# Kernel tuning notes

Measured on AMD Instinct MI355X. Metric: run time of the kernel, lower is better.

Reference implementation:

```python
import jax, jax.numpy as jnp
import numpy as np


def _l2norm(x):
    # matches torch F.normalize(p=2, dim=-1) with eps clamp
    return x / jnp.clip(jnp.linalg.norm(x, axis=-1, keepdims=True), 1e-12)


def setup_inputs() -> dict:
    key = jax.random.key(0)
    k1, k2 = jax.random.split(key)
    I, J, S, H = 32, 32, 256, 768
    return {
        "query_embs": jax.random.normal(k1, (I, S, H), dtype=jnp.float32),
        "key_embs": jax.random.normal(k2, (J, S, H), dtype=jnp.float32),
        "q_mask": jnp.ones((I, S), dtype=jnp.float32),
        "k_mask": jnp.ones((J, S), dtype=jnp.float32),
        "alpha_raw": jnp.asarray(0.5, dtype=jnp.float32),  # learned scalar param
    }


def reference(query_embs, key_embs, q_mask, k_mask, alpha_raw):
    # eval path: gumbel_temp=None, use_max=False, do_distance=True, exp_decay=True
    S = query_embs.shape[1]
    pos = jnp.arange(S)
    distance = jnp.abs(pos[:, None] - pos[None, :]).astype(jnp.float32)  # [S, S]
    alpha = jax.nn.softplus(alpha_raw)

    qn = _l2norm(query_embs)  # [I, S, H]
    kn = _l2norm(key_embs)    # [J, T, H]

    # cross similarity [I, J, S, T] with exponential distance decay
    sim = jnp.einsum('ish,jth->ijst', qn, kn) * jnp.exp(-alpha * distance)

    # valid pair mask [I, J, S, T]
    valid = q_mask[:, None, :, None] * k_mask[None, :, None, :]
    masked = sim * valid - (1.0 - valid) * 1e9

    p = jax.nn.softmax(masked, axis=-1)             # softmax over key tokens t
    agg = jnp.einsum('ijst,jth->ijsh', p, kn)       # soft-aligned key embedding
    scores = jnp.einsum('ish,ijsh->ijs', qn, agg)   # per-query-token score
    scores = scores * q_mask[:, None, :]
    denom = jnp.clip(jnp.sum(q_mask, axis=-1, keepdims=True), 1.0)  # [I, 1]
    return jnp.sum(scores, axis=-1) / denom         # [I, J]
```

## Files before the change

kernel.cpp:

```cpp
#include <hip/hip_runtime.h>

#define I_DIM 32
#define J_DIM 32
#define S_DIM 256
#define H_DIM 768
#define KC    32
#define NCH   (H_DIM / KC)
#define TILE_B 32768
#define WSQ_BYTES ((size_t)I_DIM * NCH * TILE_B)
#define WSK_BYTES ((size_t)J_DIM * NCH * TILE_B)

typedef _Float16 f16x8 __attribute__((ext_vector_type(8)));
typedef float    f32x16 __attribute__((ext_vector_type(16)));

static __device__ __forceinline__ unsigned short f16bits(_Float16 h) {
    union { _Float16 f; unsigned short u; } cv; cv.f = h; return cv.u;
}

__global__ __launch_bounds__(256) void li_split_kernel(
    const float* __restrict__ qe, const float* __restrict__ ke,
    char* __restrict__ wsQ, char* __restrict__ wsK)
{
    const int lane = threadIdx.x & 63;
    const int w    = threadIdx.x >> 6;
    const int r    = blockIdx.x * 4 + w;
    const bool isQ = r < I_DIM * S_DIM;
    const int row  = isQ ? r : r - I_DIM * S_DIM;
    const float* base = (isQ ? qe : ke) + (size_t)row * H_DIM;

    float4 v[3];
    v[0] = *(const float4*)(base + 4 * lane);
    v[1] = *(const float4*)(base + 4 * lane + 256);
    v[2] = *(const float4*)(base + 4 * lane + 512);
    float ss = 0.0f;
    #pragma unroll
    for (int g = 0; g < 3; ++g)
        ss += v[g].x * v[g].x + v[g].y * v[g].y + v[g].z * v[g].z + v[g].w * v[g].w;
    #pragma unroll
    for (int m = 1; m < 64; m <<= 1) ss += __shfl_xor(ss, m, 64);
    const float inv = 1.0f / fmaxf(sqrtf(ss), 1e-12f);

    const int mi  = row >> 8;
    const int s   = row & 255;
    const int r7  = s & 7;
    char* wsb = (isQ ? wsQ : wsK) + (size_t)mi * NCH * TILE_B + s * 128;

    #pragma unroll
    for (int g = 0; g < 3; ++g) {
        const int k0 = 4 * lane + 256 * g;
        const int c  = k0 >> 5;
        const int kk = k0 & 31;
        float xn[4] = {v[g].x * inv, v[g].y * inv, v[g].z * inv, v[g].w * inv};
        unsigned short hb[4], lb[4];
        #pragma unroll
        for (int e = 0; e < 4; ++e) {
            _Float16 h  = (_Float16)xn[e];
            _Float16 lo = (_Float16)(xn[e] - (float)h);
            hb[e] = f16bits(h);
            lb[e] = f16bits(lo);
        }
        char* p = wsb + (size_t)c * TILE_B + (((kk >> 3) ^ r7) << 4) + (kk & 7) * 2;
        *(uint2*)(p)        = make_uint2(hb[0] | ((unsigned)hb[1] << 16), hb[2] | ((unsigned)hb[3] << 16));
        *(uint2*)((char*)((size_t)p ^ 64)) = make_uint2(lb[0] | ((unsigned)lb[1] << 16), lb[2] | ((unsigned)lb[3] << 16));
    }
}

__global__ __launch_bounds__(512, 2) void li_mfma_kernel(
    const char* __restrict__ wsQ, const char* __restrict__ wsK,
    const float* __restrict__ qm, const float* __restrict__ km,
    const float* __restrict__ alpha_raw, float* __restrict__ out)
{
    __shared__ __align__(16) char sQ[2][TILE_B];
    __shared__ __align__(16) char sK[2][TILE_B];
    __shared__ float kmsh[256], qmsh[256];
    __shared__ float pm[256][2], pL[256][2], pW[256][2];
    __shared__ float redA[512], redB[512];

    const int tid = threadIdx.x;
    const int wid = tid >> 6;
    const int l   = tid & 63;
    const int l31 = l & 31;
    const int hi  = l >> 5;
    const int wx  = wid & 1;
    const int wy  = wid >> 1;
    const int r7  = l31 & 7;

    const int bidx = blockIdx.x;
    const int x  = bidx & 7;
    const int r0 = bidx >> 3;
    const int j  = x * 4 + (r0 & 3);
    const int i  = r0 >> 2;

    if (tid < 256) {
        kmsh[tid] = km[j * 256 + tid];
        qmsh[tid] = qm[i * 256 + tid];
    }
    const float araw  = alpha_raw[0];
    const float alpha = (araw > 20.0f) ? araw : log1pf(expf(araw));
    const float nal   = -alpha;

    const char* qbase = wsQ + (size_t)i * NCH * TILE_B;
    const char* kbase = wsK + (size_t)j * NCH * TILE_B;

    f32x16 acc[2][4];
    #pragma unroll
    for (int mr = 0; mr < 2; ++mr)
        #pragma unroll
        for (int nt = 0; nt < 4; ++nt)
            #pragma unroll
            for (int z = 0; z < 16; ++z) acc[mr][nt][z] = 0.0f;

#define STAGE(buf, c)                                                                      \
    do {                                                                                   \
        const char* qt_ = qbase + (size_t)(c) * TILE_B + wid * 4096 + l * 16;              \
        const char* kt_ = kbase + (size_t)(c) * TILE_B + wid * 4096 + l * 16;              \
        char* dq_ = sQ[buf] + wid * 4096;                                                  \
        char* dk_ = sK[buf] + wid * 4096;                                                  \
        _Pragma("unroll")                                                                  \
        for (int u = 0; u < 4; ++u)                                                        \
            __builtin_amdgcn_global_load_lds(                                              \
                (const __attribute__((address_space(1))) void*)(qt_ + u * 1024),           \
                (__attribute__((address_space(3))) void*)(dq_ + u * 1024), 16, 0, 0);      \
        _Pragma("unroll")                                                                  \
        for (int u = 0; u < 4; ++u)                                                        \
            __builtin_amdgcn_global_load_lds(                                              \
                (const __attribute__((address_space(1))) void*)(kt_ + u * 1024),           \
                (__attribute__((address_space(3))) void*)(dk_ + u * 1024), 16, 0, 0);      \
    } while (0)

    STAGE(0, 0);
    __syncthreads();

    for (int c = 0; c < NCH; ++c) {
        if (c + 1 < NCH) STAGE((c + 1) & 1, c + 1);
        const char* bQ = sQ[c & 1];
        const char* bK = sK[c & 1];
        #pragma unroll
        for (int ks = 0; ks < 2; ++ks) {
            const int soff = ((ks * 2 + hi) ^ r7) << 4;
            const int rA = wy * 64 + l31;
            const int rB = rA + 32;
            const f16x8 qhA = *(const f16x8*)(bQ + rA * 128 + soff);
            const f16x8 qlA = *(const f16x8*)(bQ + ((rA * 128 + soff) ^ 64));
            const f16x8 qhB = *(const f16x8*)(bQ + rB * 128 + soff);
            const f16x8 qlB = *(const f16x8*)(bQ + ((rB * 128 + soff) ^ 64));
            f16x8 kh[4], kl[4];
            #pragma unroll
            for (int nt = 0; nt < 4; ++nt) {
                const int rk = wx * 128 + nt * 32 + l31;
                kh[nt] = *(const f16x8*)(bK + rk * 128 + soff);
                kl[nt] = *(const f16x8*)(bK + ((rk * 128 + soff) ^ 64));
            }
            #pragma unroll
            for (int nt = 0; nt < 4; ++nt) {
                acc[0][nt] = __builtin_amdgcn_mfma_f32_32x32x16_f16(qhA, kh[nt], acc[0][nt], 0, 0, 0);
                acc[1][nt] = __builtin_amdgcn_mfma_f32_32x32x16_f16(qhB, kh[nt], acc[1][nt], 0, 0, 0);
            }
            #pragma unroll
            for (int nt = 0; nt < 4; ++nt) {
                acc[0][nt] = __builtin_amdgcn_mfma_f32_32x32x16_f16(qhA, kl[nt], acc[0][nt], 0, 0, 0);
                acc[1][nt] = __builtin_amdgcn_mfma_f32_32x32x16_f16(qhB, kl[nt], acc[1][nt], 0, 0, 0);
            }
            #pragma unroll
            for (int nt = 0; nt < 4; ++nt) {
                acc[0][nt] = __builtin_amdgcn_mfma_f32_32x32x16_f16(qlA, kh[nt], acc[0][nt], 0, 0, 0);
                acc[1][nt] = __builtin_amdgcn_mfma_f32_32x32x16_f16(qlB, kh[nt], acc[1][nt], 0, 0, 0);
            }
        }
        __syncthreads();
    }
#undef STAGE

    #pragma unroll
    for (int mrep = 0; mrep < 2; ++mrep) {
        #pragma unroll
        for (int reg = 0; reg < 16; ++reg) {
            const int srow = wy * 64 + mrep * 32 + hi * 4 + (reg & 3) + 8 * (reg >> 2);
            const float qms = qmsh[srow];
            float mv[4], cvv[4];
            float mloc = -3.0e38f;
            #pragma unroll
            for (int nt = 0; nt < 4; ++nt) {
                const int tcol = wx * 128 + nt * 32 + l31;
                const float cv = acc[mrep][nt][reg];
                int dd = srow - tcol; dd = dd < 0 ? -dd : dd;
                const float valid = qms * kmsh[tcol];
                const float m = cv * __expf(nal * (float)dd) * valid - (1.0f - valid) * 1e9f;
                mv[nt] = m; cvv[nt] = cv;
                mloc = fmaxf(mloc, m);
            }
            #pragma unroll
            for (int mm = 1; mm < 32; mm <<= 1)
                mloc = fmaxf(mloc, __shfl_xor(mloc, mm, 32));
            float L = 0.0f, W = 0.0f;
            #pragma unroll
            for (int nt = 0; nt < 4; ++nt) {
                const float e = __expf(mv[nt] - mloc);
                L += e;
                W += e * cvv[nt];
            }
            #pragma unroll
            for (int mm = 1; mm < 32; mm <<= 1) {
                L += __shfl_xor(L, mm, 32);
                W += __shfl_xor(W, mm, 32);
            }
            if (l31 == 0) {
                pm[srow][wx] = mloc;
                pL[srow][wx] = L;
                pW[srow][wx] = W;
            }
        }
    }
    __syncthreads();

    float contrib = 0.0f, qq = 0.0f;
    if (tid < 256) {
        const float m0 = pm[tid][0], m1 = pm[tid][1];
        const float M  = fmaxf(m0, m1);
        const float e0 = __expf(m0 - M), e1 = __expf(m1 - M);
        const float L  = pL[tid][0] * e0 + pL[tid][1] * e1;
        const float W  = pW[tid][0] * e0 + pW[tid][1] * e1;
        contrib = (W / L) * qmsh[tid];
        qq = qmsh[tid];
    }
    redA[tid] = contrib;
    redB[tid] = qq;
    __syncthreads();
    for (int off = 256; off > 0; off >>= 1) {
        if (tid < off) {
            redA[tid] += redA[tid + off];
            redB[tid] += redB[tid + off];
        }
        __syncthreads();
    }
    if (tid == 0) out[i * 32 + j] = redA[0] / fmaxf(redB[0], 1.0f);
}

extern "C" void kernel_launch(void* const* d_in, const int* in_sizes, int n_in,
                              void* d_out, int out_size, void* d_ws, size_t ws_size,
                              hipStream_t stream)
{
    const float* qe = (const float*)d_in[0];
    const float* ke = (const float*)d_in[1];
    const float* qm = (const float*)d_in[2];
    const float* km = (const float*)d_in[3];
    const float* al = (const float*)d_in[4];
    float* out = (float*)d_out;

    char* wsQ = (char*)d_ws;
    char* wsK = wsQ + WSQ_BYTES;

    hipLaunchKernelGGL(li_split_kernel, dim3((I_DIM + J_DIM) * S_DIM / 4), dim3(256),
                       0, stream, qe, ke, wsQ, wsK);
    hipLaunchKernelGGL(li_mfma_kernel, dim3(I_DIM * J_DIM), dim3(512), 0, stream,
                       wsQ, wsK, qm, km, al, out);
}
```

Measured before the change: 416.3 us.

## Interleave prefetch loads with MFMA phases using explicit barriers and priority

Restructures the main split-f16 GEMM loop into four phases per K-chunk. Each phase issues one slice of the next chunk's global-to-LDS loads, then LDS reads and a batch of 12 MFMAs. Explicit s_waitcnt, sched_barrier and s_barrier calls control ordering, and s_setprio raises priority around the MFMA bursts. The aim is to spread memory traffic across the compute and cut register pressure by loading only two K tiles at a time. It adds many more barriers per chunk, which could cost synchronisation overhead.

```diff
diff --git a/kernel.cpp b/kernel.cpp
--- a/kernel.cpp
+++ b/kernel.cpp
@@ -110,66 +110,121 @@
             #pragma unroll
             for (int z = 0; z < 16; ++z) acc[mr][nt][z] = 0.0f;
 
-#define STAGE(buf, c)                                                                      \
-    do {                                                                                   \
-        const char* qt_ = qbase + (size_t)(c) * TILE_B + wid * 4096 + l * 16;              \
-        const char* kt_ = kbase + (size_t)(c) * TILE_B + wid * 4096 + l * 16;              \
-        char* dq_ = sQ[buf] + wid * 4096;                                                  \
-        char* dk_ = sK[buf] + wid * 4096;                                                  \
-        _Pragma("unroll")                                                                  \
-        for (int u = 0; u < 4; ++u)                                                        \
-            __builtin_amdgcn_global_load_lds(                                              \
-                (const __attribute__((address_space(1))) void*)(qt_ + u * 1024),           \
-                (__attribute__((address_space(3))) void*)(dq_ + u * 1024), 16, 0, 0);      \
-        _Pragma("unroll")                                                                  \
-        for (int u = 0; u < 4; ++u)                                                        \
-            __builtin_amdgcn_global_load_lds(                                              \
-                (const __attribute__((address_space(1))) void*)(kt_ + u * 1024),           \
-                (__attribute__((address_space(3))) void*)(dk_ + u * 1024), 16, 0, 0);      \
+    const int sgo = wid * 4096 + l * 16;
+
+#define GLL2(buf, c, u)                                                                   \
+    do {                                                                                  \
+        __builtin_amdgcn_global_load_lds(                                                 \
+            (const __attribute__((address_space(1))) void*)                               \
+                (qbase + (size_t)(c) * TILE_B + sgo + (u) * 1024),                        \
+            (__attribute__((address_space(3))) void*)(sQ[buf] + wid * 4096 + (u) * 1024), \
+            16, 0, 0);                                                                    \
+        __builtin_amdgcn_global_load_lds(                                                 \
+            (const __attribute__((address_space(1))) void*)                               \
+                (kbase + (size_t)(c) * TILE_B + sgo + (u) * 1024),                        \
+            (__attribute__((address_space(3))) void*)(sK[buf] + wid * 4096 + (u) * 1024), \
+            16, 0, 0);                                                                    \
     } while (0)
 
-    STAGE(0, 0);
-    __syncthreads();
+#define SB() __builtin_amdgcn_sched_barrier(0)
+#define BAR() do { SB(); __builtin_amdgcn_s_barrier(); SB(); } while (0)
+#define LGKM0() do { asm volatile("s_waitcnt lgkmcnt(0)" ::: "memory"); SB(); } while (0)
+#define MFMA1(A, B, C) __builtin_amdgcn_mfma_f32_32x32x16_f16(A, B, C, 0, 0, 0)
+
+#define MFMA12(KHa, KLa, KHb, KLb, na, nb)                          \
+    do {                                                            \
+        __builtin_amdgcn_s_setprio(1);                              \
+        acc[0][na] = MFMA1(qh0, KHa, acc[0][na]);                   \
+        acc[0][nb] = MFMA1(qh0, KHb, acc[0][nb]);                   \
+        acc[1][na] = MFMA1(qh1, KHa, acc[1][na]);                   \
+        acc[1][nb] = MFMA1(qh1, KHb, acc[1][nb]);                   \
+        acc[0][na] = MFMA1(qh0, KLa, acc[0][na]);                   \
+        acc[0][nb] = MFMA1(qh0, KLb, acc[0][nb]);                   \
+        acc[1][na] = MFMA1(qh1, KLa, acc[1][na]);                   \
+        acc[1][nb] = MFMA1(qh1, KLb, acc[1][nb]);                   \
+        acc[0][na] = MFMA1(ql0, KHa, acc[0][na]);                   \
+        acc[0][nb] = MFMA1(ql0, KHb, acc[0][nb]);                   \
+        acc[1][na] = MFMA1(ql1, KHa, acc[1][na]);                   \
+        acc[1][nb] = MFMA1(ql1, KHb, acc[1][nb]);                   \
+        __builtin_amdgcn_s_setprio(0);                              \
+    } while (0)
+
+    const int rqA = (wy * 64 + l31) * 128;
+    const int rqB = rqA + 32 * 128;
+    const int rk0 = (wx * 128 + l31) * 128;
+
+    GLL2(0, 0, 0); GLL2(0, 0, 1); GLL2(0, 0, 2); GLL2(0, 0, 3);
+    asm volatile("s_waitcnt vmcnt(0)" ::: "memory");
+    BAR();
 
     for (int c = 0; c < NCH; ++c) {
-        if (c + 1 < NCH) STAGE((c + 1) & 1, c + 1);
         const char* bQ = sQ[c & 1];
         const char* bK = sK[c & 1];
-        #pragma unroll
-        for (int ks = 0; ks < 2; ++ks) {
-            const int soff = ((ks * 2 + hi) ^ r7) << 4;
-            const int rA = wy * 64 + l31;
-            const int rB = rA + 32;
-            const f16x8 qhA = *(const f16x8*)(bQ + rA * 128 + soff);
-            const f16x8 qlA = *(const f16x8*)(bQ + ((rA * 128 + soff) ^ 64));
-            const f16x8 qhB = *(const f16x8*)(bQ + rB * 128 + soff);
-            const f16x8 qlB = *(const f16x8*)(bQ + ((rB * 128 + soff) ^ 64));
-            f16x8 kh[4], kl[4];
-            #pragma unroll
-            for (int nt = 0; nt < 4; ++nt) {
-                const int rk = wx * 128 + nt * 32 + l31;
-                kh[nt] = *(const f16x8*)(bK + rk * 128 + soff);
-                kl[nt] = *(const f16x8*)(bK + ((rk * 128 + soff) ^ 64));
-            }
-            #pragma unroll
-            for (int nt = 0; nt < 4; ++nt) {
-                acc[0][nt] = __builtin_amdgcn_mfma_f32_32x32x16_f16(qhA, kh[nt], acc[0][nt], 0, 0, 0);
-                acc[1][nt] = __builtin_amdgcn_mfma_f32_32x32x16_f16(qhB, kh[nt], acc[1][nt], 0, 0, 0);
-            }
-            #pragma unroll
-            for (int nt = 0; nt < 4; ++nt) {
-                acc[0][nt] = __builtin_amdgcn_mfma_f32_32x32x16_f16(qhA, kl[nt], acc[0][nt], 0, 0, 0);
-                acc[1][nt] = __builtin_amdgcn_mfma_f32_32x32x16_f16(qhB, kl[nt], acc[1][nt], 0, 0, 0);
-            }
-            #pragma unroll
-            for (int nt = 0; nt < 4; ++nt) {
-                acc[0][nt] = __builtin_amdgcn_mfma_f32_32x32x16_f16(qlA, kh[nt], acc[0][nt], 0, 0, 0);
-                acc[1][nt] = __builtin_amdgcn_mfma_f32_32x32x16_f16(qlB, kh[nt], acc[1][nt], 0, 0, 0);
-            }
-        }
-        __syncthreads();
-    }
-#undef STAGE
+        const int nb = (c + 1) & 1;
+        const bool pf = (c + 1 < NCH);
+
+        f16x8 qh0, ql0, qh1, ql1;
+        f16x8 kh_a, kl_a, kh_b, kl_b;
+
+        {
+            const int soff = (hi ^ r7) << 4;
+            if (pf) {
+                GLL2(nb, c + 1, 0);
+                asm volatile("s_waitcnt vmcnt(2)" ::: "memory");
+            } else {
+                asm volatile("s_waitcnt vmcnt(0)" ::: "memory");
+            }
+            BAR();
+            qh0 = *(const f16x8*)(bQ + rqA + soff);
+            ql0 = *(const f16x8*)(bQ + ((rqA + soff) ^ 64));
+            qh1 = *(const f16x8*)(bQ + rqB + soff);
+            ql1 = *(const f16x8*)(bQ + ((rqB + soff) ^ 64));
+            kh_a = *(const f16x8*)(bK + rk0 + soff);
+            kl_a = *(const f16x8*)(bK + ((rk0 + soff) ^ 64));
+            kh_b = *(const f16x8*)(bK + rk0 + 32 * 128 + soff);
+            kl_b = *(const f16x8*)(bK + ((rk0 + 32 * 128 + soff) ^ 64));
+            LGKM0();
+            MFMA12(kh_a, kl_a, kh_b, kl_b, 0, 1);
+            BAR();
+            if (pf) GLL2(nb, c + 1, 1);
+            kh_a = *(const f16x8*)(bK + rk0 + 64 * 128 + soff);
+            kl_a = *(const f16x8*)(bK + ((rk0 + 64 * 128 + soff) ^ 64));
+            kh_b = *(const f16x8*)(bK + rk0 + 96 * 128 + soff);
+            kl_b = *(const f16x8*)(bK + ((rk0 + 96 * 128 + soff) ^ 64));
+            BAR();
+            LGKM0();
+            MFMA12(kh_a, kl_a, kh_b, kl_b, 2, 3);
+            BAR();
+        }
+        {
+            const int soff = ((2 + hi) ^ r7) << 4;
+            if (pf) GLL2(nb, c + 1, 2);
+            qh0 = *(const f16x8*)(bQ + rqA + soff);
+            ql0 = *(const f16x8*)(bQ + ((rqA + soff) ^ 64));
+            qh1 = *(const f16x8*)(bQ + rqB + soff);
+            ql1 = *(const f16x8*)(bQ + ((rqB + soff) ^ 64));
+            kh_a = *(const f16x8*)(bK + rk0 + soff);
+            kl_a = *(const f16x8*)(bK + ((rk0 + soff) ^ 64));
+            kh_b = *(const f16x8*)(bK + rk0 + 32 * 128 + soff);
+            kl_b = *(const f16x8*)(bK + ((rk0 + 32 * 128 + soff) ^ 64));
+            BAR();
+            LGKM0();
+            MFMA12(kh_a, kl_a, kh_b, kl_b, 0, 1);
+            BAR();
+            if (pf) GLL2(nb, c + 1, 3);
+            kh_a = *(const f16x8*)(bK + rk0 + 64 * 128 + soff);
+            kl_a = *(const f16x8*)(bK + ((rk0 + 64 * 128 + soff) ^ 64));
+            kh_b = *(const f16x8*)(bK + rk0 + 96 * 128 + soff);
+            kl_b = *(const f16x8*)(bK + ((rk0 + 96 * 128 + soff) ^ 64));
+            BAR();
+            LGKM0();
+            MFMA12(kh_a, kl_a, kh_b, kl_b, 2, 3);
+            BAR();
+        }
+    }
+#undef GLL2
+#undef MFMA12
+#undef MFMA1
 
     #pragma unroll
     for (int mrep = 0; mrep < 2; ++mrep) {
```

New measurement: 497.5 us. 19.5% more time.
